# Performance work log

Hardware: AMD Instinct MI355X
Metric: run time of the kernel (lower is better)

## Reference

```python
import jax, jax.numpy as jnp
import numpy as np

B, N, C, H = 8, 4096, 768, 8
EPS = 1e-12  # F.normalize eps


def setup_inputs() -> dict:
    key = jax.random.key(0)
    k1, k2, k3, k4 = jax.random.split(key, 4)
    x = jax.random.normal(k1, (B, N, C), dtype=jnp.float32)
    Wqkv = jax.random.normal(k2, (C, 3 * C), dtype=jnp.float32) * (1.0 / np.sqrt(C))
    temperature = jnp.ones((H, 1, 1), dtype=jnp.float32)
    Wproj = jax.random.normal(k3, (C, C), dtype=jnp.float32) * (1.0 / np.sqrt(C))
    bproj = jax.random.normal(k4, (C,), dtype=jnp.float32) * 0.01
    return {"x": x, "Wqkv": Wqkv, "temperature": temperature, "Wproj": Wproj, "bproj": bproj}


def _l2norm(t):
    # F.normalize(dim=-1): t / max(||t||_2, eps)
    n = jnp.sqrt(jnp.sum(t * t, axis=-1, keepdims=True))
    return t / jnp.maximum(n, EPS)


def reference(x, Wqkv, temperature, Wproj, bproj):
    b, n, c = x.shape
    h = temperature.shape[0]
    hd = c // h
    qkv = x @ Wqkv  # [B, N, 3C]
    qkv = qkv.reshape(b, n, 3, h, hd).transpose(2, 0, 3, 4, 1)  # [3, B, H, hd, N]
    q, k, v = qkv[0], qkv[1], qkv[2]
    q = _l2norm(q)  # normalize over token dim N
    k = _l2norm(k)
    # channel-channel attention: [B, H, hd, hd]
    attn = jnp.einsum('bhdn,bhen->bhde', q, k) * temperature  # temperature [H,1,1] broadcasts
    attn = jax.nn.softmax(attn, axis=-1)
    out = jnp.einsum('bhde,bhen->bhdn', attn, v)  # [B, H, hd, N]
    out = out.transpose(0, 3, 1, 2).reshape(b, n, c)  # [B, N, C]
    return out @ Wproj + bproj
```

## Files before the change

kernel.cpp:

```cpp
#include <hip/hip_runtime.h>
#include <stdint.h>


typedef __attribute__((ext_vector_type(8))) __bf16 bf16x8;
typedef __attribute__((ext_vector_type(4))) float f32x4;

__device__ __forceinline__ unsigned short f2b(float f) {
  uint32_t u = __float_as_uint(f);
  u += 0x7FFF + ((u >> 16) & 1);
  return (unsigned short)(u >> 16);
}

__device__ __forceinline__ void gload16(const void* g, void* l) {
  __builtin_amdgcn_global_load_lds(
      (__attribute__((address_space(1))) void*)(uintptr_t)g,
      (__attribute__((address_space(3))) void*)(uintptr_t)l, 16, 0, 0);
}

__global__ void cvt_bf16(const float* __restrict__ in, unsigned short* __restrict__ out, int n4,
                         float* __restrict__ Z, int nz4) {
  int gid = blockIdx.x * blockDim.x + threadIdx.x;
  if (gid < nz4) reinterpret_cast<float4*>(Z)[gid] = make_float4(0.f, 0.f, 0.f, 0.f);
  int stride = gridDim.x * blockDim.x;
  for (int i = gid; i < n4; i += stride) {
    float4 v = reinterpret_cast<const float4*>(in)[i];
    ushort4 o;
    o.x = f2b(v.x); o.y = f2b(v.y); o.z = f2b(v.z); o.w = f2b(v.w);
    reinterpret_cast<ushort4*>(out)[i] = o;
  }
}

__global__ void cvt_transpose(const float* __restrict__ in, unsigned short* __restrict__ out,
                              int K, int NC) {
  __shared__ float tile[32][33];
  int bx = blockIdx.x, by = blockIdx.y;
  int tx = threadIdx.x & 31, ty = threadIdx.x >> 5;
  for (int r = ty; r < 32; r += 8)
    tile[r][tx] = in[(size_t)(by * 32 + r) * NC + bx * 32 + tx];
  __syncthreads();
  for (int r = ty; r < 32; r += 8)
    out[(size_t)(bx * 32 + r) * K + by * 32 + tx] = f2b(tile[tx][r]);
}


#define BARX() asm volatile("s_barrier" ::: "memory")
#define WAITV(N) asm volatile("s_waitcnt vmcnt(" #N ")" ::: "memory")
#define SCHED() __builtin_amdgcn_sched_barrier(0)

#define STAGE(gbase, p, isB, h, t) do {                                             \
  unsigned short* _lb = &lds[(p)*32768 + (isB)*16384 + (h)*8192 + wid*1024];        \
  const unsigned short* _gb = (gbase) + (size_t)((h)*128 + wid*16)*768 + (t)*64 + lanegoff; \
  gload16(_gb, _lb);                                                                \
  gload16(_gb + 8*768, _lb + 512);                                                  \
} while (0)

#define LOAD_A(p, mh) do {                                                          \
  const unsigned short* _ab = &lds[(p)*32768 + (mh)*8192];                          \
  _Pragma("unroll") for (int _mi = 0; _mi < 4; _mi++)                               \
    _Pragma("unroll") for (int _kk = 0; _kk < 2; _kk++)                             \
      af[_mi][_kk] = *(const bf16x8*)&_ab[(wm*64 + _mi*16 + l16)*64 + ((_kk*4+quad)^(l16&7))*8]; \
} while (0)

#define LOAD_B(dst, p, nh) do {                                                     \
  const unsigned short* _bb = &lds[(p)*32768 + 16384 + (nh)*8192];                  \
  _Pragma("unroll") for (int _ni = 0; _ni < 2; _ni++)                               \
    _Pragma("unroll") for (int _kk = 0; _kk < 2; _kk++)                             \
      dst[_ni][_kk] = *(const bf16x8*)&_bb[(wn*32 + _ni*16 + l16)*64 + ((_kk*4+quad)^(l16&7))*8]; \
} while (0)

#define MFMA_PH(mh, nh, bfx) do {                                                   \
  __builtin_amdgcn_s_setprio(1);                                                    \
  _Pragma("unroll") for (int _m = 0; _m < 4; _m++)                                  \
    _Pragma("unroll") for (int _n = 0; _n < 2; _n++)                                \
      _Pragma("unroll") for (int _k = 0; _k < 2; _k++)                              \
        acc[(mh)*4+_m][(nh)*2+_n] = __builtin_amdgcn_mfma_f32_16x16x32_bf16(        \
            af[_m][_k], bfx[_n][_k], acc[(mh)*4+_m][(nh)*2+_n], 0, 0, 0);           \
  __builtin_amdgcn_s_setprio(0);                                                    \
} while (0)

__global__ __launch_bounds__(512, 2) void gemm_qkv(
    const unsigned short* __restrict__ A, const unsigned short* __restrict__ Bt,
    unsigned short* __restrict__ qkT, unsigned short* __restrict__ vT,
    float* __restrict__ normsq) {
  __shared__ __align__(16) unsigned short lds[65536];
  int lin = blockIdx.y * 9 + blockIdx.x;
  int swz = (lin & 7) * 144 + (lin >> 3);
  int bm = swz / 9;
  int bj = swz - bm * 9;
  int m0 = bm * 256, j0 = bj * 256;
  int tid = threadIdx.x;
  int wid = tid >> 6, lane = tid & 63;
  int wm = wid >> 2, wn = wid & 3;
  int quad = lane >> 4, l16 = lane & 15;
  int srow = lane >> 3, sch = lane & 7;
  int cmem = sch ^ srow;
  int lanegoff = srow * 768 + cmem * 8;

  f32x4 acc[8][4];
  f32x4 z = {0.f, 0.f, 0.f, 0.f};
#pragma unroll
  for (int i = 0; i < 8; i++)
#pragma unroll
    for (int j = 0; j < 4; j++) acc[i][j] = z;

  bf16x8 af[4][2], bf0[2][2], bf1[2][2];

  const unsigned short* Ab2 = A + (size_t)m0 * 768;
  const unsigned short* Bb2 = Bt + (size_t)j0 * 768;

  STAGE(Ab2, 0, 0, 0, 0); STAGE(Bb2, 0, 1, 0, 0); STAGE(Bb2, 0, 1, 1, 0); STAGE(Ab2, 0, 0, 1, 0);
  STAGE(Ab2, 1, 0, 0, 1); STAGE(Bb2, 1, 1, 0, 1); STAGE(Bb2, 1, 1, 1, 1);
  WAITV(10);
  BARX();
  LOAD_A(0, 0);
  LOAD_B(bf0, 0, 0);
  WAITV(8);
  BARX();

  for (int t = 0; t < 10; t++) {
    int p = t & 1;
    LOAD_B(bf1, p, 1);
    STAGE(Ab2, p ^ 1, 0, 1, t + 1);
    BARX(); SCHED();
    MFMA_PH(0, 0, bf0);
    SCHED(); WAITV(8); BARX();
    STAGE(Ab2, p, 0, 0, t + 2);
    BARX(); SCHED();
    MFMA_PH(0, 1, bf1);
    SCHED();
    LOAD_A(p, 1);
    BARX();
    STAGE(Bb2, p, 1, 0, t + 2);
    BARX(); SCHED();
    MFMA_PH(1, 1, bf1);
    SCHED(); WAITV(8); BARX();
    STAGE(Bb2, p, 1, 1, t + 2);
    BARX(); SCHED();
    MFMA_PH(1, 0, bf0);
    SCHED();
    LOAD_A(p ^ 1, 0);
    LOAD_B(bf0, p ^ 1, 0);
    WAITV(8); BARX();
  }
  LOAD_B(bf1, 0, 1);
  STAGE(Ab2, 1, 0, 1, 11);
  BARX(); SCHED(); MFMA_PH(0, 0, bf0); SCHED(); WAITV(8); BARX();
  BARX(); SCHED(); MFMA_PH(0, 1, bf1); SCHED(); LOAD_A(0, 1); BARX();
  BARX(); SCHED(); MFMA_PH(1, 1, bf1); SCHED(); WAITV(4); BARX();
  BARX(); SCHED(); MFMA_PH(1, 0, bf0); SCHED(); LOAD_A(1, 0); LOAD_B(bf0, 1, 0); WAITV(2); BARX();
  LOAD_B(bf1, 1, 1);
  BARX(); SCHED(); MFMA_PH(0, 0, bf0); SCHED(); WAITV(0); BARX();
  BARX(); SCHED(); MFMA_PH(0, 1, bf1); SCHED(); LOAD_A(1, 1); BARX();
  BARX(); SCHED(); MFMA_PH(1, 1, bf1); SCHED(); BARX();
  BARX(); SCHED(); MFMA_PH(1, 0, bf0); SCHED(); BARX();

  int s = bj / 3;
  int b = m0 >> 12;
  int n0 = m0 & 4095;

  if (s < 2) {
#pragma unroll
    for (int ni = 0; ni < 4; ni++) {
      float ss = 0.f;
#pragma unroll
      for (int mi = 0; mi < 8; mi++)
#pragma unroll
        for (int r = 0; r < 4; r++) ss += acc[mi][ni][r] * acc[mi][ni][r];
      ss += __shfl_down(ss, 32, 64);
      ss += __shfl_down(ss, 16, 64);
      if (lane < 16) {
        int cc = (ni >> 1) * 128 + wn * 32 + (ni & 1) * 16 + l16;
        int local = j0 + cc - s * 768;
        int hh = local / 96, d = local - hh * 96;
        atomicAdd(&normsq[s * 6144 + (b * 8 + hh) * 96 + d], ss);
      }
    }
#pragma unroll
    for (int jh = 0; jh < 2; jh++) {
      __syncthreads();
#pragma unroll
      for (int nl = 0; nl < 2; nl++) {
        int ni = jh * 2 + nl;
        int jc = wn * 32 + nl * 16 + l16;
#pragma unroll
        for (int mi = 0; mi < 8; mi++) {
          int mrow = (mi >> 2) * 128 + wm * 64 + (mi & 3) * 16 + quad * 4;
#pragma unroll
          for (int r = 0; r < 4; r++) lds[jc * 264 + mrow + r] = f2b(acc[mi][ni][r]);
        }
      }
      __syncthreads();
#pragma unroll
      for (int it = 0; it < 8; it++) {
        int id = it * 512 + tid;
        int jr = id >> 5, mc = id & 31;
        int j = j0 + jh * 128 + jr;
        int local = j - s * 768;
        int hh = local / 96, d = local - hh * 96;
        size_t off = ((size_t)(s * 64 + b * 8 + hh) * 96 + d) * 4096 + n0 + mc * 8;
        *(uint4*)&qkT[off] = *(const uint4*)&lds[jr * 264 + mc * 8];
      }
    }
  } else {
    int j0v = j0 - 1536;
#pragma unroll
    for (int mh = 0; mh < 2; mh++) {
      __syncthreads();
#pragma unroll
      for (int ml = 0; ml < 4; ml++) {
        int mi = mh * 4 + ml;
        int mloc = wm * 64 + ml * 16 + quad * 4;
#pragma unroll
        for (int ni = 0; ni < 4; ni++) {
          int jc = (ni >> 1) * 128 + wn * 32 + (ni & 1) * 16 + l16;
#pragma unroll
          for (int r = 0; r < 4; r++) lds[(mloc + r) * 264 + jc] = f2b(acc[mi][ni][r]);
        }
      }
      __syncthreads();
#pragma unroll
      for (int it = 0; it < 8; it++) {
        int id = it * 512 + tid;
        int mr = id >> 5, ch = id & 31;
        int cp = j0v + ch * 8;
        int hh = cp / 96, e = cp - hh * 96;
        size_t off = ((size_t)(b * 8 + hh) * 4096 + (n0 + mh * 128 + mr)) * 96 + e;
        *(uint4*)&vT[off] = *(const uint4*)&lds[mr * 264 + ch * 8];
      }
    }
  }
}

__global__ __launch_bounds__(256, 2) void attn_s(const unsigned short* __restrict__ qkT,
                                                 float* __restrict__ S8) {
  __shared__ __align__(16) unsigned short lds[12288];
  int blk = blockIdx.x;
  int bh = blk >> 3, ks = blk & 7;
  const unsigned short* qb = qkT + (size_t)bh * 96 * 4096;
  const unsigned short* kb = qkT + (size_t)(64 + bh) * 96 * 4096;
  int tid = threadIdx.x, wid = tid >> 6, lane = tid & 63;
  int wm = wid >> 1, wn = wid & 1, quad = lane >> 4, l16 = lane & 15;
  int srow = lane >> 3, sch = lane & 7;
  int cmem = sch ^ srow;
  f32x4 acc[3][3];
  f32x4 z = {0.f, 0.f, 0.f, 0.f};
#pragma unroll
  for (int i = 0; i < 3; i++)
#pragma unroll
    for (int j = 0; j < 3; j++) acc[i][j] = z;

  for (int k0 = ks * 512; k0 < ks * 512 + 512; k0 += 64) {
#pragma unroll
    for (int i = 0; i < 3; i++) {
      int ig = wid * 3 + i;
      int row = ig * 8 + srow;
      gload16(qb + (size_t)row * 4096 + k0 + cmem * 8, &lds[ig * 512]);
      gload16(kb + (size_t)row * 4096 + k0 + cmem * 8, &lds[6144 + ig * 512]);
    }
    __syncthreads();
#pragma unroll
    for (int kk = 0; kk < 2; kk++) {
      int cs = ((kk * 4 + quad) ^ (l16 & 7)) * 8;
      bf16x8 af[3], bfr[3];
#pragma unroll
      for (int mi = 0; mi < 3; mi++)
        af[mi] = *(const bf16x8*)&lds[(wm * 48 + mi * 16 + l16) * 64 + cs];
#pragma unroll
      for (int ni = 0; ni < 3; ni++)
        bfr[ni] = *(const bf16x8*)&lds[6144 + (wn * 48 + ni * 16 + l16) * 64 + cs];
#pragma unroll
      for (int mi = 0; mi < 3; mi++)
#pragma unroll
        for (int ni = 0; ni < 3; ni++)
          acc[mi][ni] = __builtin_amdgcn_mfma_f32_16x16x32_bf16(af[mi], bfr[ni], acc[mi][ni], 0, 0, 0);
    }
    __syncthreads();
  }
  float* Sb = S8 + ((size_t)ks * 64 + bh) * 9216;
#pragma unroll
  for (int mi = 0; mi < 3; mi++)
#pragma unroll
    for (int ni = 0; ni < 3; ni++)
#pragma unroll
      for (int r = 0; r < 4; r++)
        Sb[(wm * 48 + mi * 16 + quad * 4 + r) * 96 + wn * 48 + ni * 16 + l16] = acc[mi][ni][r];
}

__global__ __launch_bounds__(256) void softmax96(
    const float* __restrict__ S8, const float* __restrict__ normsq,
    const float* __restrict__ temp, unsigned short* __restrict__ attnB) {
  __shared__ float Sl[24][97];
  __shared__ float ik[96], iqv[24];
  int part = blockIdx.x;
  int bh = blockIdx.y;
  int h = bh & 7;
  int base = part * 24;
  int tid = threadIdx.x;
  if (tid < 96) {
    ik[tid] = 1.0f / fmaxf(sqrtf(normsq[6144 + bh * 96 + tid]), 1e-12f);
  } else if (tid >= 128 && tid < 152) {
    int d = base + tid - 128;
    iqv[tid - 128] = (1.0f / fmaxf(sqrtf(normsq[bh * 96 + d]), 1e-12f)) * temp[h];
  }
  const float* Sbase = S8 + (size_t)bh * 9216 + base * 96;
#pragma unroll
  for (int i = 0; i < 9; i++) {
    int idx = i * 256 + tid;
    int r = idx / 96, e = idx - r * 96;
    float s = 0.f;
#pragma unroll
    for (int ksb = 0; ksb < 8; ksb++) s += Sbase[(size_t)ksb * 589824 + r * 96 + e];
    Sl[r][e] = s;
  }
  __syncthreads();
  int wv = tid >> 6, lane = tid & 63;
  for (int r = wv; r < 24; r += 4) {
    float iq = iqv[r];
    float v0 = Sl[r][lane] * iq * ik[lane];
    float v1 = (lane < 32) ? Sl[r][64 + lane] * iq * ik[64 + lane] : -1e30f;
    float mx = fmaxf(v0, v1);
#pragma unroll
    for (int off = 32; off; off >>= 1) mx = fmaxf(mx, __shfl_xor(mx, off, 64));
    float e0 = __expf(v0 - mx);
    float e1 = (lane < 32) ? __expf(v1 - mx) : 0.f;
    float sm = e0 + e1;
#pragma unroll
    for (int off = 32; off; off >>= 1) sm += __shfl_xor(sm, off, 64);
    float inv = 1.0f / sm;
    unsigned short* row = attnB + (size_t)bh * 9984 + (base + r) * 104;
    row[lane] = f2b(e0 * inv);
    if (lane < 32) row[64 + lane] = f2b(e1 * inv);
    else if (64 + lane < 104) row[64 + lane] = 0;
  }
}

__global__ __launch_bounds__(256, 4) void attn_v(
    const unsigned short* __restrict__ attnB, const unsigned short* __restrict__ vT,
    unsigned short* __restrict__ U) {
  __shared__ __align__(16) unsigned short lds[23552];
  int blk = blockIdx.x;
  int bh = blk >> 5, nc = blk & 31;
  int b = bh >> 3, h = bh & 7;
  int n0 = nc * 128;
  int tid = threadIdx.x, wid = tid >> 6, lane = tid & 63;
  int wm = wid >> 1, wn = wid & 1, quad = lane >> 4, l16 = lane & 15;

  const unsigned short* ab = attnB + (size_t)bh * 9984;
#pragma unroll
  for (int i = 0; i < 5; i++) {
    int id = i * 256 + tid;
    int ids = id < 1248 ? id : 1247;
    gload16(ab + (size_t)ids * 8, &lds[(i * 4 + wid) * 512]);
  }

  const unsigned short* vb = vT + (size_t)bh * 4096 * 96 + (size_t)n0 * 96;
#pragma unroll
  for (int i = 0; i < 7; i++) {
    int ig = wid + i * 4;
    if (ig < 26) {
      int id = ig * 64 + lane;
      int row = id / 13;
      int ch = id - row * 13;
      if (ch > 11) ch = 11;
      gload16(vb + (size_t)row * 96 + ch * 8, &lds[10240 + ig * 512]);
    }
  }
  __syncthreads();

  f32x4 acc[3][4];
  f32x4 z = {0.f, 0.f, 0.f, 0.f};
#pragma unroll
  for (int i = 0; i < 3; i++)
#pragma unroll
    for (int j = 0; j < 4; j++) acc[i][j] = z;
#pragma unroll
  for (int et = 0; et < 3; et++) {
    bf16x8 af[3], bfr[4];
#pragma unroll
    for (int mi = 0; mi < 3; mi++)
      af[mi] = *(const bf16x8*)&lds[(wm * 48 + mi * 16 + l16) * 104 + (et * 4 + quad) * 8];
#pragma unroll
    for (int ni = 0; ni < 4; ni++)
      bfr[ni] = *(const bf16x8*)&lds[10240 + (wn * 64 + ni * 16 + l16) * 104 + (et * 4 + quad) * 8];
#pragma unroll
    for (int mi = 0; mi < 3; mi++)
#pragma unroll
      for (int ni = 0; ni < 4; ni++)
        acc[mi][ni] = __builtin_amdgcn_mfma_f32_16x16x32_bf16(af[mi], bfr[ni], acc[mi][ni], 0, 0, 0);
  }
  __syncthreads();

#pragma unroll
  for (int mi = 0; mi < 3; mi++)
#pragma unroll
    for (int ni = 0; ni < 4; ni++)
#pragma unroll
      for (int r = 0; r < 4; r++) {
        int d = wm * 48 + mi * 16 + quad * 4 + r;
        int n = wn * 64 + ni * 16 + l16;
        lds[n * 104 + d] = f2b(acc[mi][ni][r]);
      }
  __syncthreads();
#pragma unroll
  for (int it = 0; it < 6; it++) {
    int id = tid + it * 256;
    int nr = id / 12, ch = id - nr * 12;
    *(uint4*)&U[((size_t)(b * 4096 + n0 + nr)) * 768 + h * 96 + ch * 8] =
        *(const uint4*)&lds[nr * 104 + ch * 8];
  }
}

__global__ __launch_bounds__(256, 2) void gemm_out(
    const unsigned short* __restrict__ A, const unsigned short* __restrict__ Bt,
    const float* __restrict__ bias, float* __restrict__ out) {
  __shared__ __align__(16) unsigned short lds[16384];
  int bj = blockIdx.x;
  int bm = blockIdx.y;
  int m0 = bm * 128, j0 = bj * 128;
  int tid = threadIdx.x;
  int wid = tid >> 6, lane = tid & 63;
  int wm = wid >> 1, wn = wid & 1;
  int quad = lane >> 4, l16 = lane & 15;
  int srow = lane >> 3, sch = lane & 7;
  int cmem = sch ^ srow;

  f32x4 acc[4][4];
  f32x4 z = {0.f, 0.f, 0.f, 0.f};
#pragma unroll
  for (int i = 0; i < 4; i++)
#pragma unroll
    for (int j = 0; j < 4; j++) acc[i][j] = z;

  const unsigned short* Ab = A + (size_t)m0 * 768;
  const unsigned short* Bb = Bt + (size_t)j0 * 768;

  for (int k0 = 0; k0 < 768; k0 += 64) {
#pragma unroll
    for (int i = 0; i < 4; i++) {
      int ig = wid * 4 + i;
      int row = ig * 8 + srow;
      gload16(Ab + (size_t)row * 768 + k0 + cmem * 8, &lds[ig * 512]);
      gload16(Bb + (size_t)row * 768 + k0 + cmem * 8, &lds[8192 + ig * 512]);
    }
    __syncthreads();
#pragma unroll
    for (int kk = 0; kk < 2; kk++) {
      int cs = ((kk * 4 + quad) ^ (l16 & 7)) * 8;
      bf16x8 af[4], bfr[4];
#pragma unroll
      for (int mi = 0; mi < 4; mi++)
        af[mi] = *(const bf16x8*)&lds[(wm * 64 + mi * 16 + l16) * 64 + cs];
#pragma unroll
      for (int ni = 0; ni < 4; ni++)
        bfr[ni] = *(const bf16x8*)&lds[8192 + (wn * 64 + ni * 16 + l16) * 64 + cs];
#pragma unroll
      for (int mi = 0; mi < 4; mi++)
#pragma unroll
        for (int ni = 0; ni < 4; ni++)
          acc[mi][ni] = __builtin_amdgcn_mfma_f32_16x16x32_bf16(af[mi], bfr[ni], acc[mi][ni], 0, 0, 0);
    }
    __syncthreads();
  }
#pragma unroll
  for (int ni = 0; ni < 4; ni++) {
    int ccol = j0 + wn * 64 + ni * 16 + l16;
    float bv = bias[ccol];
#pragma unroll
    for (int mi = 0; mi < 4; mi++)
#pragma unroll
      for (int r = 0; r < 4; r++)
        out[(size_t)(m0 + wm * 64 + mi * 16 + quad * 4 + r) * 768 + ccol] = acc[mi][ni][r] + bv;
  }
}

extern "C" void kernel_launch(void* const* d_in, const int* in_sizes, int n_in,
                              void* d_out, int out_size, void* d_ws, size_t ws_size,
                              hipStream_t stream) {
  const float* x = (const float*)d_in[0];
  const float* Wqkv = (const float*)d_in[1];
  const float* temp = (const float*)d_in[2];
  const float* Wproj = (const float*)d_in[3];
  const float* bproj = (const float*)d_in[4];
  float* out = (float*)d_out;
  char* ws = (char*)d_ws;

  unsigned short* xb     = (unsigned short*)(ws);
  unsigned short* WqkvT  = (unsigned short*)(ws + 50331648);
  unsigned short* WprojT = (unsigned short*)(ws + 53870592);
  unsigned short* qkT    = (unsigned short*)(ws + 55050240);
  unsigned short* vT     = (unsigned short*)(ws + 155713536);
  unsigned short* U      = (unsigned short*)(ws + 206045184);
  float* normsq          = (float*)(ws + 258736128);
  float* S8              = (float*)(ws);
  unsigned short* attnB  = qkT;

  cvt_bf16<<<dim3(4096), dim3(256), 0, stream>>>(x, xb, 25165824 / 4, normsq, 3072);
  cvt_transpose<<<dim3(72, 24), dim3(256), 0, stream>>>(Wqkv, WqkvT, 768, 2304);
  cvt_transpose<<<dim3(24, 24), dim3(256), 0, stream>>>(Wproj, WprojT, 768, 768);
  gemm_qkv<<<dim3(9, 128), dim3(512), 0, stream>>>(xb, WqkvT, qkT, vT, normsq);
  attn_s<<<dim3(512), dim3(256), 0, stream>>>(qkT, S8);
  softmax96<<<dim3(4, 64), dim3(256), 0, stream>>>(S8, normsq, temp, attnB);
  attn_v<<<dim3(2048), dim3(256), 0, stream>>>(attnB, vT, U);
  gemm_out<<<dim3(6, 256), dim3(256), 0, stream>>>(U, WprojT, bproj, out);
}
```

Before: 426.4 us.

## Compute Q·K^T and norms via Gram matrix X^T X instead of materializing Q,K

Replaces the Q/K projection GEMM and the N-length Q·K^T reduction with an algebraic route: G = X^T X per batch (768x768), then T = G·Wq/Wk, and S = Wq^T G Wk computed per head alongside the squared norms as diagonal terms. This avoids writing and re-reading the large qkT tensor and the split-K partial-sum buffer, and leaves only the V projection as a full-N GEMM. The cost is an extra transposed bf16 copy of x, a non-pipelined Gram GEMM, and a softmax kernel with only 64 blocks. It also changes numerical rounding because G and T are stored in bf16.

Result: slower. 464.7 us (+9.0%).

```diff
diff --git a/kernel.cpp b/kernel.cpp
--- a/kernel.cpp
+++ b/kernel.cpp
@@ -17,17 +17,31 @@
       (__attribute__((address_space(3))) void*)(uintptr_t)l, 16, 0, 0);
 }
 
-__global__ void cvt_bf16(const float* __restrict__ in, unsigned short* __restrict__ out, int n4,
-                         float* __restrict__ Z, int nz4) {
-  int gid = blockIdx.x * blockDim.x + threadIdx.x;
-  if (gid < nz4) reinterpret_cast<float4*>(Z)[gid] = make_float4(0.f, 0.f, 0.f, 0.f);
-  int stride = gridDim.x * blockDim.x;
-  for (int i = gid; i < n4; i += stride) {
-    float4 v = reinterpret_cast<const float4*>(in)[i];
-    ushort4 o;
-    o.x = f2b(v.x); o.y = f2b(v.y); o.z = f2b(v.z); o.w = f2b(v.w);
-    reinterpret_cast<ushort4*>(out)[i] = o;
-  }
+__device__ __forceinline__ float dot8(const unsigned short* a, const unsigned short* b) {
+  uint4 va = *(const uint4*)a, vb = *(const uint4*)b;
+  const unsigned short* pa = (const unsigned short*)&va;
+  const unsigned short* pb = (const unsigned short*)&vb;
+  float s = 0.f;
+#pragma unroll
+  for (int i = 0; i < 8; i++)
+    s += __uint_as_float((uint32_t)pa[i] << 16) * __uint_as_float((uint32_t)pb[i] << 16);
+  return s;
+}
+
+__global__ void cvt_x(const float* __restrict__ in, unsigned short* __restrict__ xb,
+                      unsigned short* __restrict__ xbT) {
+  __shared__ float tile[32][33];
+  int bx = blockIdx.x, by = blockIdx.y, b = blockIdx.z;
+  int tx = threadIdx.x & 31, ty = threadIdx.x >> 5;
+  const float* src = in + (size_t)b * 4096 * 768;
+  for (int r = ty; r < 32; r += 8) {
+    float v = src[(size_t)(by * 32 + r) * 768 + bx * 32 + tx];
+    tile[r][tx] = v;
+    xb[((size_t)b * 4096 + by * 32 + r) * 768 + bx * 32 + tx] = f2b(v);
+  }
+  __syncthreads();
+  for (int r = ty; r < 32; r += 8)
+    xbT[((size_t)b * 768 + bx * 32 + r) * 4096 + by * 32 + tx] = f2b(tile[tx][r]);
 }
 
 __global__ void cvt_transpose(const float* __restrict__ in, unsigned short* __restrict__ out,
@@ -41,7 +55,6 @@
   for (int r = ty; r < 32; r += 8)
     out[(size_t)(bx * 32 + r) * K + by * 32 + tx] = f2b(tile[tx][r]);
 }
-
 
 #define BARX() asm volatile("s_barrier" ::: "memory")
 #define WAITV(N) asm volatile("s_waitcnt vmcnt(" #N ")" ::: "memory")
@@ -78,15 +91,14 @@
   __builtin_amdgcn_s_setprio(0);                                                    \
 } while (0)
 
-__global__ __launch_bounds__(512, 2) void gemm_qkv(
+__global__ __launch_bounds__(512, 2) void gemm_v(
     const unsigned short* __restrict__ A, const unsigned short* __restrict__ Bt,
-    unsigned short* __restrict__ qkT, unsigned short* __restrict__ vT,
-    float* __restrict__ normsq) {
+    unsigned short* __restrict__ vT) {
   __shared__ __align__(16) unsigned short lds[65536];
-  int lin = blockIdx.y * 9 + blockIdx.x;
-  int swz = (lin & 7) * 144 + (lin >> 3);
-  int bm = swz / 9;
-  int bj = swz - bm * 9;
+  int lin = blockIdx.y * 3 + blockIdx.x;
+  int swz = (lin & 7) * 48 + (lin >> 3);
+  int bm = swz / 3;
+  int bj = 6 + (swz - bm * 3);
   int m0 = bm * 256, j0 = bj * 256;
   int tid = threadIdx.x;
   int wid = tid >> 6, lane = tid & 63;
@@ -154,108 +166,205 @@
   BARX(); SCHED(); MFMA_PH(1, 1, bf1); SCHED(); BARX();
   BARX(); SCHED(); MFMA_PH(1, 0, bf0); SCHED(); BARX();
 
-  int s = bj / 3;
   int b = m0 >> 12;
   int n0 = m0 & 4095;
-
-  if (s < 2) {
-#pragma unroll
-    for (int ni = 0; ni < 4; ni++) {
-      float ss = 0.f;
-#pragma unroll
-      for (int mi = 0; mi < 8; mi++)
-#pragma unroll
-        for (int r = 0; r < 4; r++) ss += acc[mi][ni][r] * acc[mi][ni][r];
-      ss += __shfl_down(ss, 32, 64);
-      ss += __shfl_down(ss, 16, 64);
-      if (lane < 16) {
-        int cc = (ni >> 1) * 128 + wn * 32 + (ni & 1) * 16 + l16;
-        int local = j0 + cc - s * 768;
-        int hh = local / 96, d = local - hh * 96;
-        atomicAdd(&normsq[s * 6144 + (b * 8 + hh) * 96 + d], ss);
+  int j0v = j0 - 1536;
+#pragma unroll
+  for (int mh = 0; mh < 2; mh++) {
+    __syncthreads();
+#pragma unroll
+    for (int ml = 0; ml < 4; ml++) {
+      int mi = mh * 4 + ml;
+      int mloc = wm * 64 + ml * 16 + quad * 4;
+#pragma unroll
+      for (int ni = 0; ni < 4; ni++) {
+        int jc = (ni >> 1) * 128 + wn * 32 + (ni & 1) * 16 + l16;
+#pragma unroll
+        for (int r = 0; r < 4; r++) lds[(mloc + r) * 264 + jc] = f2b(acc[mi][ni][r]);
       }
     }
-#pragma unroll
-    for (int jh = 0; jh < 2; jh++) {
-      __syncthreads();
-#pragma unroll
-      for (int nl = 0; nl < 2; nl++) {
-        int ni = jh * 2 + nl;
-        int jc = wn * 32 + nl * 16 + l16;
-#pragma unroll
-        for (int mi = 0; mi < 8; mi++) {
-          int mrow = (mi >> 2) * 128 + wm * 64 + (mi & 3) * 16 + quad * 4;
-#pragma unroll
-          for (int r = 0; r < 4; r++) lds[jc * 264 + mrow + r] = f2b(acc[mi][ni][r]);
-        }
+    __syncthreads();
+#pragma unroll
+    for (int it = 0; it < 8; it++) {
+      int id = it * 512 + tid;
+      int mr = id >> 5, ch = id & 31;
+      int cp = j0v + ch * 8;
+      int hh = cp / 96, e = cp - hh * 96;
+      size_t off = ((size_t)(b * 8 + hh) * 4096 + (n0 + mh * 128 + mr)) * 96 + e;
+      *(uint4*)&vT[off] = *(const uint4*)&lds[mr * 264 + ch * 8];
+    }
+  }
+}
+
+__global__ __launch_bounds__(256, 2) void gemm_g(
+    const unsigned short* __restrict__ xbT, unsigned short* __restrict__ G) {
+  __shared__ __align__(16) unsigned short lds[16384];
+  int bj = blockIdx.x;
+  int bz = blockIdx.y;
+  int b = bz / 6, mt = bz - b * 6;
+  int m0 = mt * 128, j0 = bj * 128;
+  int tid = threadIdx.x;
+  int wid = tid >> 6, lane = tid & 63;
+  int wm = wid >> 1, wn = wid & 1;
+  int quad = lane >> 4, l16 = lane & 15;
+  int srow = lane >> 3, sch = lane & 7;
+  int cmem = sch ^ srow;
+
+  f32x4 acc[4][4];
+  f32x4 z = {0.f, 0.f, 0.f, 0.f};
+#pragma unroll
+  for (int i = 0; i < 4; i++)
+#pragma unroll
+    for (int j = 0; j < 4; j++) acc[i][j] = z;
+
+  const unsigned short* Ab = xbT + ((size_t)b * 768 + m0) * 4096;
+  const unsigned short* Bb = xbT + ((size_t)b * 768 + j0) * 4096;
+
+  for (int k0 = 0; k0 < 4096; k0 += 64) {
+#pragma unroll
+    for (int i = 0; i < 4; i++) {
+      int ig = wid * 4 + i;
+      int row = ig * 8 + srow;
+      gload16(Ab + (size_t)row * 4096 + k0 + cmem * 8, &lds[ig * 512]);
+      gload16(Bb + (size_t)row * 4096 + k0 + cmem * 8, &lds[8192 + ig * 512]);
+    }
+    __syncthreads();
+#pragma unroll
+    for (int kk = 0; kk < 2; kk++) {
+      int cs = ((kk * 4 + quad) ^ (l16 & 7)) * 8;
+      bf16x8 af[4], bfr[4];
+#pragma unroll
+      for (int mi = 0; mi < 4; mi++)
+        af[mi] = *(const bf16x8*)&lds[(wm * 64 + mi * 16 + l16) * 64 + cs];
+#pragma unroll
+      for (int ni = 0; ni < 4; ni++)
+        bfr[ni] = *(const bf16x8*)&lds[8192 + (wn * 64 + ni * 16 + l16) * 64 + cs];
+#pragma unroll
+      for (int mi = 0; mi < 4; mi++)
+#pragma unroll
+        for (int ni = 0; ni < 4; ni++)
+          acc[mi][ni] = __builtin_amdgcn_mfma_f32_16x16x32_bf16(af[mi], bfr[ni], acc[mi][ni], 0, 0, 0);
+    }
+    __syncthreads();
+  }
+  unsigned short* Gb = G + ((size_t)b * 768 + m0) * 768 + j0;
+#pragma unroll
+  for (int ni = 0; ni < 4; ni++)
+#pragma unroll
+    for (int mi = 0; mi < 4; mi++)
+#pragma unroll
+      for (int r = 0; r < 4; r++)
+        Gb[(size_t)(wm * 64 + mi * 16 + quad * 4 + r) * 768 + wn * 64 + ni * 16 + l16] =
+            f2b(acc[mi][ni][r]);
+}
+
+__global__ __launch_bounds__(256, 2) void gemm_t12(
+    const unsigned short* __restrict__ G, const unsigned short* __restrict__ WqkvT,
+    unsigned short* __restrict__ T12t) {
+  __shared__ __align__(16) unsigned short lds[17408];
+  int bj = blockIdx.x;
+  int bz = blockIdx.y;
+  int b = bz / 6, mt = bz - b * 6;
+  int m0 = mt * 128, j0 = bj * 128;
+  int tid = threadIdx.x;
+  int wid = tid >> 6, lane = tid & 63;
+  int wm = wid >> 1, wn = wid & 1;
+  int quad = lane >> 4, l16 = lane & 15;
+  int srow = lane >> 3, sch = lane & 7;
+  int cmem = sch ^ srow;
+
+  f32x4 acc[4][4];
+  f32x4 z = {0.f, 0.f, 0.f, 0.f};
+#pragma unroll
+  for (int i = 0; i < 4; i++)
+#pragma unroll
+    for (int j = 0; j < 4; j++) acc[i][j] = z;
+
+  const unsigned short* Ab = G + ((size_t)b * 768 + m0) * 768;
+  const unsigned short* Bb = WqkvT + (size_t)j0 * 768;
+
+  for (int k0 = 0; k0 < 768; k0 += 64) {
+#pragma unroll
+    for (int i = 0; i < 4; i++) {
+      int ig = wid * 4 + i;
+      int row = ig * 8 + srow;
+      gload16(Ab + (size_t)row * 768 + k0 + cmem * 8, &lds[ig * 512]);
+      gload16(Bb + (size_t)row * 768 + k0 + cmem * 8, &lds[8192 + ig * 512]);
+    }
+    __syncthreads();
+#pragma unroll
+    for (int kk = 0; kk < 2; kk++) {
+      int cs = ((kk * 4 + quad) ^ (l16 & 7)) * 8;
+      bf16x8 af[4], bfr[4];
+#pragma unroll
+      for (int mi = 0; mi < 4; mi++)
+        af[mi] = *(const bf16x8*)&lds[(wm * 64 + mi * 16 + l16) * 64 + cs];
+#pragma unroll
+      for (int ni = 0; ni < 4; ni++)
+        bfr[ni] = *(const bf16x8*)&lds[8192 + (wn * 64 + ni * 16 + l16) * 64 + cs];
+#pragma unroll
+      for (int mi = 0; mi < 4; mi++)
+#pragma unroll
+        for (int ni = 0; ni < 4; ni++)
+          acc[mi][ni] = __builtin_amdgcn_mfma_f32_16x16x32_bf16(af[mi], bfr[ni], acc[mi][ni], 0, 0, 0);
+    }
+    __syncthreads();
+  }
+#pragma unroll
+  for (int mi = 0; mi < 4; mi++)
+#pragma unroll
+    for (int ni = 0; ni < 4; ni++)
+#pragma unroll
+      for (int r = 0; r < 4; r++) {
+        int m = wm * 64 + mi * 16 + quad * 4 + r;
+        int cc = wn * 64 + ni * 16 + l16;
+        lds[cc * 136 + m] = f2b(acc[mi][ni][r]);
       }
-      __syncthreads();
-#pragma unroll
-      for (int it = 0; it < 8; it++) {
-        int id = it * 512 + tid;
-        int jr = id >> 5, mc = id & 31;
-        int j = j0 + jh * 128 + jr;
-        int local = j - s * 768;
-        int hh = local / 96, d = local - hh * 96;
-        size_t off = ((size_t)(s * 64 + b * 8 + hh) * 96 + d) * 4096 + n0 + mc * 8;
-        *(uint4*)&qkT[off] = *(const uint4*)&lds[jr * 264 + mc * 8];
-      }
-    }
-  } else {
-    int j0v = j0 - 1536;
-#pragma unroll
-    for (int mh = 0; mh < 2; mh++) {
-      __syncthreads();
-#pragma unroll
-      for (int ml = 0; ml < 4; ml++) {
-        int mi = mh * 4 + ml;
-        int mloc = wm * 64 + ml * 16 + quad * 4;
-#pragma unroll
-        for (int ni = 0; ni < 4; ni++) {
-          int jc = (ni >> 1) * 128 + wn * 32 + (ni & 1) * 16 + l16;
-#pragma unroll
-          for (int r = 0; r < 4; r++) lds[(mloc + r) * 264 + jc] = f2b(acc[mi][ni][r]);
-        }
-      }
-      __syncthreads();
-#pragma unroll
-      for (int it = 0; it < 8; it++) {
-        int id = it * 512 + tid;
-        int mr = id >> 5, ch = id & 31;
-        int cp = j0v + ch * 8;
-        int hh = cp / 96, e = cp - hh * 96;
-        size_t off = ((size_t)(b * 8 + hh) * 4096 + (n0 + mh * 128 + mr)) * 96 + e;
-        *(uint4*)&vT[off] = *(const uint4*)&lds[mr * 264 + ch * 8];
-      }
-    }
-  }
-}
-
-__global__ __launch_bounds__(256, 2) void attn_s(const unsigned short* __restrict__ qkT,
-                                                 float* __restrict__ S8) {
-  __shared__ __align__(16) unsigned short lds[12288];
-  int blk = blockIdx.x;
-  int bh = blk >> 3, ks = blk & 7;
-  const unsigned short* qb = qkT + (size_t)bh * 96 * 4096;
-  const unsigned short* kb = qkT + (size_t)(64 + bh) * 96 * 4096;
+  __syncthreads();
+#pragma unroll
+  for (int it = 0; it < 8; it++) {
+    int id = tid + it * 256;
+    int jr = id >> 4, mc = id & 15;
+    *(uint4*)&T12t[((size_t)b * 1536 + j0 + jr) * 768 + m0 + mc * 8] =
+        *(const uint4*)&lds[jr * 136 + mc * 8];
+  }
+}
+
+__global__ __launch_bounds__(256, 2) void softmax_s(
+    const unsigned short* __restrict__ T12t, const unsigned short* __restrict__ WqkvT,
+    const float* __restrict__ temp, unsigned short* __restrict__ attnB) {
+  __shared__ __align__(16) unsigned short lds[24960];
+  float* nq = (float*)&lds[24576];
+  float* nk = (float*)&lds[24768];
+  int bh = blockIdx.x;
+  int b = bh >> 3, h = bh & 7;
   int tid = threadIdx.x, wid = tid >> 6, lane = tid & 63;
   int wm = wid >> 1, wn = wid & 1, quad = lane >> 4, l16 = lane & 15;
-  int srow = lane >> 3, sch = lane & 7;
-  int cmem = sch ^ srow;
+  int srow = lane >> 3, sch = lane & 7, cmem = sch ^ srow;
+
+  const unsigned short* pb0 = T12t + ((size_t)b * 1536 + h * 96) * 768;
+  const unsigned short* pb1 = WqkvT + (size_t)(h * 96) * 768;
+  const unsigned short* pb2 = T12t + ((size_t)b * 1536 + 768 + h * 96) * 768;
+  const unsigned short* pb3 = WqkvT + (size_t)(768 + h * 96) * 768;
+
   f32x4 acc[3][3];
   f32x4 z = {0.f, 0.f, 0.f, 0.f};
 #pragma unroll
   for (int i = 0; i < 3; i++)
 #pragma unroll
     for (int j = 0; j < 3; j++) acc[i][j] = z;
-
-  for (int k0 = ks * 512; k0 < ks * 512 + 512; k0 += 64) {
+  float aq[3] = {0.f, 0.f, 0.f}, ak[3] = {0.f, 0.f, 0.f};
+
+  for (int k0 = 0; k0 < 768; k0 += 64) {
 #pragma unroll
     for (int i = 0; i < 3; i++) {
-      int ig = wid * 3 + i;
-      int row = ig * 8 + srow;
-      gload16(qb + (size_t)row * 4096 + k0 + cmem * 8, &lds[ig * 512]);
-      gload16(kb + (size_t)row * 4096 + k0 + cmem * 8, &lds[6144 + ig * 512]);
+      int igrp = wid * 3 + i;
+      int row = igrp * 8 + srow;
+      size_t off = (size_t)row * 768 + k0 + cmem * 8;
+      gload16(pb0 + off, &lds[igrp * 512]);
+      gload16(pb1 + off, &lds[6144 + igrp * 512]);
+      gload16(pb2 + off, &lds[12288 + igrp * 512]);
+      gload16(pb3 + off, &lds[18432 + igrp * 512]);
     }
     __syncthreads();
 #pragma unroll
@@ -267,57 +376,45 @@
         af[mi] = *(const bf16x8*)&lds[(wm * 48 + mi * 16 + l16) * 64 + cs];
 #pragma unroll
       for (int ni = 0; ni < 3; ni++)
-        bfr[ni] = *(const bf16x8*)&lds[6144 + (wn * 48 + ni * 16 + l16) * 64 + cs];
+        bfr[ni] = *(const bf16x8*)&lds[18432 + (wn * 48 + ni * 16 + l16) * 64 + cs];
 #pragma unroll
       for (int mi = 0; mi < 3; mi++)
 #pragma unroll
         for (int ni = 0; ni < 3; ni++)
           acc[mi][ni] = __builtin_amdgcn_mfma_f32_16x16x32_bf16(af[mi], bfr[ni], acc[mi][ni], 0, 0, 0);
     }
-    __syncthreads();
-  }
-  float* Sb = S8 + ((size_t)ks * 64 + bh) * 9216;
+#pragma unroll
+    for (int s = 0; s < 3; s++) {
+      int idx = s * 256 + tid;
+      int r = idx >> 3, ch = idx & 7;
+      aq[s] += dot8(&lds[r * 64 + ch * 8], &lds[6144 + r * 64 + ch * 8]);
+      ak[s] += dot8(&lds[12288 + r * 64 + ch * 8], &lds[18432 + r * 64 + ch * 8]);
+    }
+    __syncthreads();
+  }
+#pragma unroll
+  for (int s = 0; s < 3; s++) {
+    float vq = aq[s], vk = ak[s];
+    vq += __shfl_down(vq, 4, 8); vq += __shfl_down(vq, 2, 8); vq += __shfl_down(vq, 1, 8);
+    vk += __shfl_down(vk, 4, 8); vk += __shfl_down(vk, 2, 8); vk += __shfl_down(vk, 1, 8);
+    if ((tid & 7) == 0) { nq[s * 32 + (tid >> 3)] = vq; nk[s * 32 + (tid >> 3)] = vk; }
+  }
+  __syncthreads();
+  float* Sf = (float*)lds;
 #pragma unroll
   for (int mi = 0; mi < 3; mi++)
 #pragma unroll
     for (int ni = 0; ni < 3; ni++)
 #pragma unroll
       for (int r = 0; r < 4; r++)
-        Sb[(wm * 48 + mi * 16 + quad * 4 + r) * 96 + wn * 48 + ni * 16 + l16] = acc[mi][ni][r];
-}
-
-__global__ __launch_bounds__(256) void softmax96(
-    const float* __restrict__ S8, const float* __restrict__ normsq,
-    const float* __restrict__ temp, unsigned short* __restrict__ attnB) {
-  __shared__ float Sl[24][97];
-  __shared__ float ik[96], iqv[24];
-  int part = blockIdx.x;
-  int bh = blockIdx.y;
-  int h = bh & 7;
-  int base = part * 24;
-  int tid = threadIdx.x;
-  if (tid < 96) {
-    ik[tid] = 1.0f / fmaxf(sqrtf(normsq[6144 + bh * 96 + tid]), 1e-12f);
-  } else if (tid >= 128 && tid < 152) {
-    int d = base + tid - 128;
-    iqv[tid - 128] = (1.0f / fmaxf(sqrtf(normsq[bh * 96 + d]), 1e-12f)) * temp[h];
-  }
-  const float* Sbase = S8 + (size_t)bh * 9216 + base * 96;
-#pragma unroll
-  for (int i = 0; i < 9; i++) {
-    int idx = i * 256 + tid;
-    int r = idx / 96, e = idx - r * 96;
-    float s = 0.f;
-#pragma unroll
-    for (int ksb = 0; ksb < 8; ksb++) s += Sbase[(size_t)ksb * 589824 + r * 96 + e];
-    Sl[r][e] = s;
-  }
-  __syncthreads();
-  int wv = tid >> 6, lane = tid & 63;
-  for (int r = wv; r < 24; r += 4) {
-    float iq = iqv[r];
-    float v0 = Sl[r][lane] * iq * ik[lane];
-    float v1 = (lane < 32) ? Sl[r][64 + lane] * iq * ik[64 + lane] : -1e30f;
+        Sf[(wm * 48 + mi * 16 + quad * 4 + r) * 97 + wn * 48 + ni * 16 + l16] = acc[mi][ni][r];
+  if (tid < 96) nk[tid] = 1.0f / fmaxf(sqrtf(nk[tid]), 1e-12f);
+  __syncthreads();
+  float tval = temp[h];
+  for (int r = wid; r < 96; r += 4) {
+    float iq = tval / fmaxf(sqrtf(nq[r]), 1e-12f);
+    float v0 = Sf[r * 97 + lane] * iq * nk[lane];
+    float v1 = (lane < 32) ? Sf[r * 97 + 64 + lane] * iq * nk[64 + lane] : -1e30f;
     float mx = fmaxf(v0, v1);
 #pragma unroll
     for (int off = 32; off; off >>= 1) mx = fmaxf(mx, __shfl_xor(mx, off, 64));
@@ -327,7 +424,7 @@
 #pragma unroll
     for (int off = 32; off; off >>= 1) sm += __shfl_xor(sm, off, 64);
     float inv = 1.0f / sm;
-    unsigned short* row = attnB + (size_t)bh * 9984 + (base + r) * 104;
+    unsigned short* row = attnB + (size_t)bh * 9984 + r * 104;
     row[lane] = f2b(e0 * inv);
     if (lane < 32) row[64 + lane] = f2b(e1 * inv);
     else if (64 + lane < 104) row[64 + lane] = 0;
@@ -487,19 +584,20 @@
   unsigned short* xb     = (unsigned short*)(ws);
   unsigned short* WqkvT  = (unsigned short*)(ws + 50331648);
   unsigned short* WprojT = (unsigned short*)(ws + 53870592);
-  unsigned short* qkT    = (unsigned short*)(ws + 55050240);
-  unsigned short* vT     = (unsigned short*)(ws + 155713536);
-  unsigned short* U      = (unsigned short*)(ws + 206045184);
-  float* normsq          = (float*)(ws + 258736128);
-  float* S8              = (float*)(ws);
-  unsigned short* attnB  = qkT;
-
-  cvt_bf16<<<dim3(4096), dim3(256), 0, stream>>>(x, xb, 25165824 / 4, normsq, 3072);
+  unsigned short* xbT    = (unsigned short*)(ws + 55050240);
+  unsigned short* vT     = (unsigned short*)(ws + 105381888);
+  unsigned short* U      = (unsigned short*)(ws + 155713536);
+  unsigned short* G      = (unsigned short*)(ws + 206045184);
+  unsigned short* T12t   = (unsigned short*)(ws + 215482368);
+  unsigned short* attnB  = (unsigned short*)(ws + 234356736);
+
+  cvt_x<<<dim3(24, 128, 8), dim3(256), 0, stream>>>(x, xb, xbT);
   cvt_transpose<<<dim3(72, 24), dim3(256), 0, stream>>>(Wqkv, WqkvT, 768, 2304);
   cvt_transpose<<<dim3(24, 24), dim3(256), 0, stream>>>(Wproj, WprojT, 768, 768);
-  gemm_qkv<<<dim3(9, 128), dim3(512), 0, stream>>>(xb, WqkvT, qkT, vT, normsq);
-  attn_s<<<dim3(512), dim3(256), 0, stream>>>(qkT, S8);
-  softmax96<<<dim3(4, 64), dim3(256), 0, stream>>>(S8, normsq, temp, attnB);
+  gemm_g<<<dim3(6, 48), dim3(256), 0, stream>>>(xbT, G);
+  gemm_t12<<<dim3(12, 48), dim3(256), 0, stream>>>(G, WqkvT, T12t);
+  softmax_s<<<dim3(64), dim3(256), 0, stream>>>(T12t, WqkvT, temp, attnB);
+  gemm_v<<<dim3(3, 128), dim3(512), 0, stream>>>(xb, WqkvT, vT);
   attn_v<<<dim3(2048), dim3(256), 0, stream>>>(attnB, vT, U);
   gemm_out<<<dim3(6, 256), dim3(256), 0, stream>>>(U, WprojT, bproj, out);
 }
```
